# Kernel tuning notes

Measured on AMD Instinct MI355X. Metric: run time of the kernel, lower is better.

Reference implementation:

```python
import jax, jax.numpy as jnp
import numpy as np
from jax import lax

WINDOW = 11
SIGMA = 1.5
CHANNELS = 3
DATA_RANGE = 1.0
WEIGHTS = (0.0448, 0.2856, 0.3001, 0.2363, 0.1333)


def _gaussian_kernel_2d(size, sigma, channels):
    x = np.arange(size, dtype=np.float32) - size // 2
    k1 = np.exp(-x ** 2 / (2 * sigma ** 2))
    k1 = k1 / k1.sum()
    k2 = np.outer(k1, k1)
    k2 = k2 / k2.sum()
    return jnp.asarray(np.tile(k2[None, None], (channels, 1, 1, 1)), dtype=jnp.float32)


def _depthwise_blur(x, kernel):
    # x: [B, G, H, W], kernel: [C, 1, kh, kw] tiled to G groups
    groups = x.shape[1]
    reps = groups // kernel.shape[0]
    k = jnp.tile(kernel, (reps, 1, 1, 1))
    return lax.conv_general_dilated(
        x, k, window_strides=(1, 1), padding='SAME',
        feature_group_count=groups,
        dimension_numbers=('NCHW', 'OIHW', 'NCHW'))


def _avg_pool2(x):
    b, c, h, w = x.shape
    return x.reshape(b, c, h // 2, 2, w // 2, 2).mean(axis=(3, 5))


def _ssim_components(pred, target, kernel):
    C1 = (0.01 * DATA_RANGE) ** 2
    C2 = (0.03 * DATA_RANGE) ** 2
    # Fuse the 5 depthwise blurs into a single grouped conv over stacked channels
    stacked = jnp.concatenate(
        [pred, target, pred * pred, target * target, pred * target], axis=1)
    blurred = _depthwise_blur(stacked, kernel)
    mu1, mu2, e_pp, e_tt, e_pt = jnp.split(blurred, 5, axis=1)
    mu1_sq = mu1 * mu1
    mu2_sq = mu2 * mu2
    mu1_mu2 = mu1 * mu2
    sigma1_sq = jnp.maximum(e_pp - mu1_sq, 0.0)
    sigma2_sq = jnp.maximum(e_tt - mu2_sq, 0.0)
    sigma12 = e_pt - mu1_mu2
    l = (2 * mu1_mu2 + C1) / (mu1_sq + mu2_sq + C1)
    cs = (2 * sigma12 + C2) / (sigma1_sq + sigma2_sq + C2)
    return l.mean(), cs.mean()


def setup_inputs() -> dict:
    key = jax.random.key(0)
    k1, k2 = jax.random.split(key)
    pred = jax.random.uniform(k1, (16, 3, 512, 512), dtype=jnp.float32)
    target = jax.random.uniform(k2, (16, 3, 512, 512), dtype=jnp.float32)
    kernel = _gaussian_kernel_2d(WINDOW, SIGMA, CHANNELS)
    return {'pred': pred, 'target': target, 'kernel': kernel}


def reference(pred, target, kernel):
    weights = jnp.asarray(WEIGHTS, dtype=pred.dtype)
    msssim = jnp.ones((1,), dtype=pred.dtype)
    n_scales = len(WEIGHTS)
    for i in range(n_scales):
        if i > 0:
            pred = _avg_pool2(pred)
            target = _avg_pool2(target)
        if pred.shape[2] < WINDOW or pred.shape[3] < WINDOW:
            break
        l, cs = _ssim_components(pred, target, kernel)
        if i == n_scales - 1:
            msssim = msssim * jnp.maximum(l, 1e-8) ** weights[i] \
                            * jnp.maximum(cs, 1e-8) ** weights[i]
        else:
            msssim = msssim * jnp.maximum(cs, 1e-8) ** weights[i]
    return msssim
```

## Files before the change

### kernel.cpp

```cpp
#include <hip/hip_runtime.h>
#include <math.h>

#define NP 48

typedef float v2f __attribute__((ext_vector_type(2)));

__global__ __launch_bounds__(256) void k_poolall(
        const float* __restrict__ p0, const float* __restrict__ t0,
        float* __restrict__ p1, float* __restrict__ t1,
        float* __restrict__ p2, float* __restrict__ t2,
        float* __restrict__ p3, float* __restrict__ t3,
        float* __restrict__ p4, float* __restrict__ t4) {
    __shared__ float l1[16][17];
    __shared__ float l2[8][9];
    __shared__ float l3[4][5];
    int t    = threadIdx.x;
    int tile = blockIdx.x;
    int pl   = blockIdx.y;
    int z    = blockIdx.z;
    int tY = tile >> 4, tX = tile & 15;

    const float* src = z ? t0 : p0;
    float* d1 = z ? t1 : p1;
    float* d2 = z ? t2 : p2;
    float* d3 = z ? t3 : p3;
    float* d4 = z ? t4 : p4;

    int ty = t >> 4, tx = t & 15;
    int y1 = tY * 16 + ty, x1 = tX * 16 + tx;
    size_t b0 = (size_t)pl * 512 * 512 + (size_t)(2 * y1) * 512 + 2 * x1;
    float2 r0 = *(const float2*)(src + b0);
    float2 r1 = *(const float2*)(src + b0 + 512);
    float v1 = 0.25f * ((r0.x + r0.y) + (r1.x + r1.y));
    d1[(size_t)pl * 256 * 256 + (size_t)y1 * 256 + x1] = v1;
    l1[ty][tx] = v1;
    __syncthreads();
    if (t < 64) {
        int y = t >> 3, x = t & 7;
        float v2 = 0.25f * (l1[2*y][2*x] + l1[2*y][2*x+1] + l1[2*y+1][2*x] + l1[2*y+1][2*x+1]);
        d2[(size_t)pl * 128 * 128 + (size_t)(tY*8 + y) * 128 + (tX*8 + x)] = v2;
        l2[y][x] = v2;
    }
    __syncthreads();
    if (t < 16) {
        int y = t >> 2, x = t & 3;
        float v3 = 0.25f * (l2[2*y][2*x] + l2[2*y][2*x+1] + l2[2*y+1][2*x] + l2[2*y+1][2*x+1]);
        d3[(size_t)pl * 64 * 64 + (size_t)(tY*4 + y) * 64 + (tX*4 + x)] = v3;
        l3[y][x] = v3;
    }
    __syncthreads();
    if (t < 4) {
        int y = t >> 1, x = t & 1;
        float v4 = 0.25f * (l3[2*y][2*x] + l3[2*y][2*x+1] + l3[2*y+1][2*x] + l3[2*y+1][2*x+1]);
        d4[(size_t)pl * 32 * 32 + (size_t)(tY*2 + y) * 32 + (tX*2 + x)] = v4;
    }
}

__global__ __launch_bounds__(256) void k_ssim_all(
        const float* __restrict__ pred, const float* __restrict__ targ,
        const float* __restrict__ p1, const float* __restrict__ t1,
        const float* __restrict__ p2, const float* __restrict__ t2,
        const float* __restrict__ p3, const float* __restrict__ t3,
        const float* __restrict__ p4, const float* __restrict__ t4,
        const float* __restrict__ k2d, double* __restrict__ accum) {
    int b   = blockIdx.x;
    int tid = threadIdx.x;
    const float *P, *T;
    int H, sh, base, scale;
    if (b < 1536)      { scale = 0; H = 512; sh = 9; base = 0;    P = pred; T = targ; }
    else if (b < 1920) { scale = 1; H = 256; sh = 8; base = 1536; P = p1;   T = t1;   }
    else if (b < 2016) { scale = 2; H = 128; sh = 7; base = 1920; P = p2;   T = t2;   }
    else if (b < 2040) { scale = 3; H = 64;  sh = 6; base = 2016; P = p3;   T = t3;   }
    else               { scale = 4; H = 32;  sh = 5; base = 2040; P = p4;   T = t4;   }
    int lb      = b - base;
    int blocksX = (NP << sh) >> 8;
    int bxi = lb % blocksX;
    int by  = lb / blocksX;
    int g   = (bxi << 8) + tid;
    int pl  = g >> sh;
    int x   = g & (H - 1);
    int yb  = by * 32;
    int yend = yb + 32;

    float w[11];
    {
        float s = 0.f;
#pragma unroll
        for (int i = 0; i < 11; ++i) s += k2d[55 + i];
        float inv = 1.0f / s;
#pragma unroll
        for (int i = 0; i < 11; ++i) w[i] = k2d[55 + i] * inv;
    }

    const float* Pp = P + (size_t)pl * H * H;
    const float* Tp = T + (size_t)pl * H * H;

    int bcl = x - 5;
    bcl = bcl < 0 ? 0 : bcl;
    bcl = bcl > H - 11 ? H - 11 : bcl;
    int d = bcl - (x - 5);
    v2f wc2[11];
#pragma unroll
    for (int j = 0; j < 11; ++j) {
        int idx = j + d;
        float val = 0.f;
#pragma unroll
        for (int i = 0; i < 11; ++i) val = (idx == i) ? w[i] : val;
        wc2[j] = (v2f){val, val};
    }
    v2f w2v[11];
#pragma unroll
    for (int i = 0; i < 11; ++i) w2v[i] = (v2f){w[i], w[i]};

    v2f wmu[11], we[11];
    float wpt[11];
    const float C1 = 1e-4f, C2 = 9e-4f;
    float lsum = 0.f, csum = 0.f;

    int rr = yb - 5;
    const float* pP = Pp + (ptrdiff_t)rr * H + bcl;
    const float* pT = Tp + (ptrdiff_t)rr * H + bcl;

    for (int ch = 0; ch < 4; ++ch) {
#pragma unroll
        for (int ph = 0; ph < 11; ++ph) {
            bool live = rr < yend + 5;
            v2f a_mu = (v2f){0.f, 0.f};
            v2f a_e  = (v2f){0.f, 0.f};
            float a_pt = 0.f;
            if (live && rr >= 0 && rr < H) {
#pragma unroll
                for (int j = 0; j < 11; ++j) {
                    v2f pt2 = (v2f){pP[j], pT[j]};
                    v2f wp2 = wc2[j] * pt2;
                    a_mu += wp2;
                    a_e  += wp2 * pt2;
                    a_pt += wp2.x * pt2.y;
                }
            }
            wmu[ph] = a_mu; we[ph] = a_e; wpt[ph] = a_pt;
            if (live && rr >= yb + 5) {
                v2f mu2 = (v2f){0.f, 0.f};
                v2f e2  = (v2f){0.f, 0.f};
                float ept = 0.f;
#pragma unroll
                for (int i = 0; i < 11; ++i) {
                    const int sl = (ph + 1 + i) % 11;
                    mu2 += w2v[i] * wmu[sl];
                    e2  += w2v[i] * we[sl];
                    ept += w[i] * wpt[sl];
                }
                float m11 = mu2.x * mu2.x, m22 = mu2.y * mu2.y, m12 = mu2.x * mu2.y;
                float s1  = fmaxf(e2.x - m11, 0.f);
                float s2  = fmaxf(e2.y - m22, 0.f);
                float s12 = ept - m12;
                lsum += (2.f * m12 + C1) * __builtin_amdgcn_rcpf(m11 + m22 + C1);
                csum += (2.f * s12 + C2) * __builtin_amdgcn_rcpf(s1 + s2 + C2);
            }
            rr++; pP += H; pT += H;
        }
    }

#pragma unroll
    for (int o = 32; o > 0; o >>= 1) {
        lsum += __shfl_down(lsum, o, 64);
        csum += __shfl_down(csum, o, 64);
    }
    __shared__ float red[8];
    int wv = tid >> 6;
    if ((tid & 63) == 0) { red[2 * wv] = lsum; red[2 * wv + 1] = csum; }
    __syncthreads();
    if (tid == 0) {
        int slot = (scale * 8 + (b & 7)) * 2;
        atomicAdd(&accum[slot],     (double)(red[0] + red[2] + red[4] + red[6]));
        atomicAdd(&accum[slot + 1], (double)(red[1] + red[3] + red[5] + red[7]));
    }
}

__global__ void k_final(const double* __restrict__ accum, float* __restrict__ out) {
    if (threadIdx.x != 0 || blockIdx.x != 0) return;
    const double wts[5] = {0.0448, 0.2856, 0.3001, 0.2363, 0.1333};
    double ms = 1.0;
    int Hs = 512;
    for (int s = 0; s < 5; ++s) {
        double lt = 0.0, ct = 0.0;
        for (int k = 0; k < 8; ++k) {
            lt += accum[(s * 8 + k) * 2];
            ct += accum[(s * 8 + k) * 2 + 1];
        }
        double N  = 48.0 * (double)Hs * (double)Hs;
        double l  = lt / N;
        double cs = ct / N;
        if (cs < 1e-8) cs = 1e-8;
        if (s == 4) {
            if (l < 1e-8) l = 1e-8;
            ms *= pow(l, wts[s]) * pow(cs, wts[s]);
        } else {
            ms *= pow(cs, wts[s]);
        }
        Hs >>= 1;
    }
    out[0] = (float)ms;
}

extern "C" void kernel_launch(void* const* d_in, const int* in_sizes, int n_in,
                              void* d_out, int out_size, void* d_ws, size_t ws_size,
                              hipStream_t stream) {
    const float* pred = (const float*)d_in[0];
    const float* targ = (const float*)d_in[1];
    const float* kern = (const float*)d_in[2];
    float* out = (float*)d_out;

    char* ws = (char*)d_ws;
    double* accum = (double*)ws;
    size_t off = 1024;
    float* p1 = (float*)(ws + off); off += (size_t)NP * 256 * 256 * 4;
    float* t1 = (float*)(ws + off); off += (size_t)NP * 256 * 256 * 4;
    float* p2 = (float*)(ws + off); off += (size_t)NP * 128 * 128 * 4;
    float* t2 = (float*)(ws + off); off += (size_t)NP * 128 * 128 * 4;
    float* p3 = (float*)(ws + off); off += (size_t)NP * 64 * 64 * 4;
    float* t3 = (float*)(ws + off); off += (size_t)NP * 64 * 64 * 4;
    float* p4 = (float*)(ws + off); off += (size_t)NP * 32 * 32 * 4;
    float* t4 = (float*)(ws + off); off += (size_t)NP * 32 * 32 * 4;

    hipMemsetAsync(accum, 0, 640, stream);
    k_poolall<<<dim3(256, NP, 2), 256, 0, stream>>>(pred, targ, p1, t1, p2, t2, p3, t3, p4, t4);
    k_ssim_all<<<2046, 256, 0, stream>>>(pred, targ, p1, t1, p2, t2, p3, t3, p4, t4, kern, accum);
    k_final<<<1, 1, 0, stream>>>(accum, out);
}
```

Baseline: 237.9 us.

## Fuse pyramid pooling with full-res SSIM and run coarse scales afterwards

Restructures the kernel schedule. Pooling of the whole pyramid now runs in the same launch as the full-resolution SSIM blocks, since scale 0 does not depend on the pooled outputs, and a second launch handles scales 1-4. The pooling is rewritten so each thread reduces an 8x8 patch in registers with float4 loads and shuffles instead of shared-memory stages. The aim is to overlap the pooling traffic with the dominant scale-0 compute and remove a launch dependency, at the cost of a mixed-role grid that may balance unevenly.

Measured after the change: 237.2 us. Within noise of the previous version (-0.3%).

```diff
diff --git a/kernel.cpp b/kernel.cpp
--- a/kernel.cpp
+++ b/kernel.cpp
@@ -5,74 +5,21 @@
 
 typedef float v2f __attribute__((ext_vector_type(2)));
 
-__global__ __launch_bounds__(256) void k_poolall(
-        const float* __restrict__ p0, const float* __restrict__ t0,
-        float* __restrict__ p1, float* __restrict__ t1,
-        float* __restrict__ p2, float* __restrict__ t2,
-        float* __restrict__ p3, float* __restrict__ t3,
-        float* __restrict__ p4, float* __restrict__ t4) {
-    __shared__ float l1[16][17];
-    __shared__ float l2[8][9];
-    __shared__ float l3[4][5];
-    int t    = threadIdx.x;
-    int tile = blockIdx.x;
-    int pl   = blockIdx.y;
-    int z    = blockIdx.z;
-    int tY = tile >> 4, tX = tile & 15;
-
-    const float* src = z ? t0 : p0;
-    float* d1 = z ? t1 : p1;
-    float* d2 = z ? t2 : p2;
-    float* d3 = z ? t3 : p3;
-    float* d4 = z ? t4 : p4;
-
-    int ty = t >> 4, tx = t & 15;
-    int y1 = tY * 16 + ty, x1 = tX * 16 + tx;
-    size_t b0 = (size_t)pl * 512 * 512 + (size_t)(2 * y1) * 512 + 2 * x1;
-    float2 r0 = *(const float2*)(src + b0);
-    float2 r1 = *(const float2*)(src + b0 + 512);
-    float v1 = 0.25f * ((r0.x + r0.y) + (r1.x + r1.y));
-    d1[(size_t)pl * 256 * 256 + (size_t)y1 * 256 + x1] = v1;
-    l1[ty][tx] = v1;
-    __syncthreads();
-    if (t < 64) {
-        int y = t >> 3, x = t & 7;
-        float v2 = 0.25f * (l1[2*y][2*x] + l1[2*y][2*x+1] + l1[2*y+1][2*x] + l1[2*y+1][2*x+1]);
-        d2[(size_t)pl * 128 * 128 + (size_t)(tY*8 + y) * 128 + (tX*8 + x)] = v2;
-        l2[y][x] = v2;
-    }
-    __syncthreads();
-    if (t < 16) {
-        int y = t >> 2, x = t & 3;
-        float v3 = 0.25f * (l2[2*y][2*x] + l2[2*y][2*x+1] + l2[2*y+1][2*x] + l2[2*y+1][2*x+1]);
-        d3[(size_t)pl * 64 * 64 + (size_t)(tY*4 + y) * 64 + (tX*4 + x)] = v3;
-        l3[y][x] = v3;
-    }
-    __syncthreads();
-    if (t < 4) {
-        int y = t >> 1, x = t & 1;
-        float v4 = 0.25f * (l3[2*y][2*x] + l3[2*y][2*x+1] + l3[2*y+1][2*x] + l3[2*y+1][2*x+1]);
-        d4[(size_t)pl * 32 * 32 + (size_t)(tY*2 + y) * 32 + (tX*2 + x)] = v4;
-    }
-}
-
-__global__ __launch_bounds__(256) void k_ssim_all(
-        const float* __restrict__ pred, const float* __restrict__ targ,
-        const float* __restrict__ p1, const float* __restrict__ t1,
-        const float* __restrict__ p2, const float* __restrict__ t2,
-        const float* __restrict__ p3, const float* __restrict__ t3,
-        const float* __restrict__ p4, const float* __restrict__ t4,
-        const float* __restrict__ k2d, double* __restrict__ accum) {
-    int b   = blockIdx.x;
-    int tid = threadIdx.x;
-    const float *P, *T;
-    int H, sh, base, scale;
-    if (b < 1536)      { scale = 0; H = 512; sh = 9; base = 0;    P = pred; T = targ; }
-    else if (b < 1920) { scale = 1; H = 256; sh = 8; base = 1536; P = p1;   T = t1;   }
-    else if (b < 2016) { scale = 2; H = 128; sh = 7; base = 1920; P = p2;   T = t2;   }
-    else if (b < 2040) { scale = 3; H = 64;  sh = 6; base = 2016; P = p3;   T = t3;   }
-    else               { scale = 4; H = 32;  sh = 5; base = 2040; P = p4;   T = t4;   }
-    int lb      = b - base;
+__device__ __forceinline__ void ssim_scale(
+        const float* __restrict__ P, const float* __restrict__ T,
+        int H, int sh, int lb, int scale, int slotsel, int tid,
+        const float* __restrict__ k2d, double* __restrict__ accum)
+{
+    float w[11];
+    {
+        float s = 0.f;
+#pragma unroll
+        for (int i = 0; i < 11; ++i) s += k2d[55 + i];
+        float inv = 1.0f / s;
+#pragma unroll
+        for (int i = 0; i < 11; ++i) w[i] = k2d[55 + i] * inv;
+    }
+
     int blocksX = (NP << sh) >> 8;
     int bxi = lb % blocksX;
     int by  = lb / blocksX;
@@ -81,16 +28,6 @@
     int x   = g & (H - 1);
     int yb  = by * 32;
     int yend = yb + 32;
-
-    float w[11];
-    {
-        float s = 0.f;
-#pragma unroll
-        for (int i = 0; i < 11; ++i) s += k2d[55 + i];
-        float inv = 1.0f / s;
-#pragma unroll
-        for (int i = 0; i < 11; ++i) w[i] = k2d[55 + i] * inv;
-    }
 
     const float* Pp = P + (size_t)pl * H * H;
     const float* Tp = T + (size_t)pl * H * H;
@@ -171,10 +108,81 @@
     if ((tid & 63) == 0) { red[2 * wv] = lsum; red[2 * wv + 1] = csum; }
     __syncthreads();
     if (tid == 0) {
-        int slot = (scale * 8 + (b & 7)) * 2;
+        int slot = (scale * 8 + slotsel) * 2;
         atomicAdd(&accum[slot],     (double)(red[0] + red[2] + red[4] + red[6]));
         atomicAdd(&accum[slot + 1], (double)(red[1] + red[3] + red[5] + red[7]));
     }
+}
+
+__global__ __launch_bounds__(256) void k_main(
+        const float* __restrict__ pred, const float* __restrict__ targ,
+        float* __restrict__ p1, float* __restrict__ t1,
+        float* __restrict__ p2, float* __restrict__ t2,
+        float* __restrict__ p3, float* __restrict__ t3,
+        float* __restrict__ p4, float* __restrict__ t4,
+        const float* __restrict__ k2d, double* __restrict__ accum) {
+    int b   = blockIdx.x;
+    int tid = threadIdx.x;
+    if (b >= 1536) {
+        ssim_scale(pred, targ, 512, 9, b - 1536, 0, b & 7, tid, k2d, accum);
+        return;
+    }
+    int pi   = b >> 4;
+    int tile = b & 15;
+    int pls  = pi < 48 ? pi : pi - 48;
+    const float* src = (pi < 48 ? pred : targ) + (size_t)pls * 512 * 512;
+    float* d1 = (pi < 48 ? p1 : t1) + (size_t)pls * 256 * 256;
+    float* d2 = (pi < 48 ? p2 : t2) + (size_t)pls * 128 * 128;
+    float* d3 = (pi < 48 ? p3 : t3) + (size_t)pls * 64 * 64;
+    float* d4 = (pi < 48 ? p4 : t4) + (size_t)pls * 32 * 32;
+    int tY = tile >> 2, tX = tile & 3;
+    int ty = tid >> 4, tx = tid & 15;
+    int gy0 = tY * 128 + ty * 8, gx0 = tX * 128 + tx * 8;
+
+    float s1v[4][4];
+#pragma unroll
+    for (int i = 0; i < 4; ++i) {
+        const float* r0 = src + (size_t)(gy0 + 2 * i) * 512 + gx0;
+        const float* r1 = r0 + 512;
+        float4 a0 = *(const float4*)r0, a1 = *(const float4*)(r0 + 4);
+        float4 b0 = *(const float4*)r1, b1 = *(const float4*)(r1 + 4);
+        s1v[i][0] = 0.25f * ((a0.x + a0.y) + (b0.x + b0.y));
+        s1v[i][1] = 0.25f * ((a0.z + a0.w) + (b0.z + b0.w));
+        s1v[i][2] = 0.25f * ((a1.x + a1.y) + (b1.x + b1.y));
+        s1v[i][3] = 0.25f * ((a1.z + a1.w) + (b1.z + b1.w));
+        *(float4*)(d1 + (size_t)(tY * 64 + ty * 4 + i) * 256 + tX * 64 + tx * 4) =
+            *(float4*)s1v[i];
+    }
+    float s2v[2][2];
+#pragma unroll
+    for (int i = 0; i < 2; ++i) {
+#pragma unroll
+        for (int j = 0; j < 2; ++j)
+            s2v[i][j] = 0.25f * ((s1v[2*i][2*j] + s1v[2*i][2*j+1]) +
+                                 (s1v[2*i+1][2*j] + s1v[2*i+1][2*j+1]));
+        *(float2*)(d2 + (size_t)(tY * 32 + ty * 2 + i) * 128 + tX * 32 + tx * 2) =
+            *(float2*)s2v[i];
+    }
+    float s3 = 0.25f * ((s2v[0][0] + s2v[0][1]) + (s2v[1][0] + s2v[1][1]));
+    d3[(size_t)(tY * 16 + ty) * 64 + tX * 16 + tx] = s3;
+    float v1 = s3 + __shfl_xor(s3, 1, 64);
+    float v2 = v1 + __shfl_xor(v1, 16, 64);
+    if ((ty & 1) == 0 && (tx & 1) == 0)
+        d4[(size_t)(tY * 8 + (ty >> 1)) * 32 + tX * 8 + (tx >> 1)] = 0.25f * v2;
+}
+
+__global__ __launch_bounds__(256) void k_ssim_rest(
+        const float* __restrict__ p1, const float* __restrict__ t1,
+        const float* __restrict__ p2, const float* __restrict__ t2,
+        const float* __restrict__ p3, const float* __restrict__ t3,
+        const float* __restrict__ p4, const float* __restrict__ t4,
+        const float* __restrict__ k2d, double* __restrict__ accum) {
+    int b   = blockIdx.x;
+    int tid = threadIdx.x;
+    if (b < 384)      ssim_scale(p1, t1, 256, 8, b,       1, b & 7, tid, k2d, accum);
+    else if (b < 480) ssim_scale(p2, t2, 128, 7, b - 384, 2, b & 7, tid, k2d, accum);
+    else if (b < 504) ssim_scale(p3, t3, 64,  6, b - 480, 3, b & 7, tid, k2d, accum);
+    else              ssim_scale(p4, t4, 32,  5, b - 504, 4, b & 7, tid, k2d, accum);
 }
 
 __global__ void k_final(const double* __restrict__ accum, float* __restrict__ out) {
@@ -224,7 +232,7 @@
     float* t4 = (float*)(ws + off); off += (size_t)NP * 32 * 32 * 4;
 
     hipMemsetAsync(accum, 0, 640, stream);
-    k_poolall<<<dim3(256, NP, 2), 256, 0, stream>>>(pred, targ, p1, t1, p2, t2, p3, t3, p4, t4);
-    k_ssim_all<<<2046, 256, 0, stream>>>(pred, targ, p1, t1, p2, t2, p3, t3, p4, t4, kern, accum);
+    k_main<<<3072, 256, 0, stream>>>(pred, targ, p1, t1, p2, t2, p3, t3, p4, t4, kern, accum);
+    k_ssim_rest<<<510, 256, 0, stream>>>(p1, t1, p2, t2, p3, t3, p4, t4, kern, accum);
     k_final<<<1, 1, 0, stream>>>(accum, out);
 }
```
